# Performance work log

Hardware: AMD Instinct MI355X
Metric: run time of the kernel (lower is better)

## Reference

```python
import jax, jax.numpy as jnp
import numpy as np

NUM_LONGTERM_MEM = 16  # config.num_longterm_mem


def setup_inputs() -> dict:
    key = jax.random.key(0)
    ks = jax.random.split(key, 9)
    B, T, C, H = 32, 2048, 768, 1536
    s = 0.02
    return {
        "x": jax.random.normal(ks[0], (B, T, C), jnp.float32),
        "Wq": jax.random.normal(ks[1], (C, C), jnp.float32) * s,
        "bq": jax.random.normal(ks[2], (C,), jnp.float32) * s,
        "W0": jax.random.normal(ks[3], (B, H, C), jnp.float32) * s,
        "b0": jax.random.normal(ks[4], (B, H), jnp.float32) * s,
        "W1": jax.random.normal(ks[5], (B, C, H), jnp.float32) * s,
        "b1": jax.random.normal(ks[6], (B, C), jnp.float32) * s,
        "Wo": jax.random.normal(ks[7], (C, C), jnp.float32) * s,
        "bo": jax.random.normal(ks[8], (C,), jnp.float32) * s,
    }


def reference(x, Wq, bq, W0, b0, W1, b1, Wo, bo):
    # x: [B, T, C]. Per-sample memory MLP weights W0 [B,H,C], W1 [B,C,H].
    B, T, C = x.shape
    L = NUM_LONGTERM_MEM
    # query projection (nn.Linear: x @ W^T + b)
    q = jnp.einsum("btc,dc->btd", x, Wq) + bq                       # [B,T,C]
    # per-sample 2-layer memory MLP with SiLU
    h = jax.nn.silu(jnp.einsum("btc,bhc->bth", q, W0) + b0[:, None, :])  # [B,T,H]
    mem = jnp.einsum("bth,bch->btc", h, W1) + b1[:, None, :]        # [B,T,C]
    # adaptive_avg_pool1d over T -> L (T divisible by L => uniform window mean)
    pooled = mem.reshape(B, L, T // L, C).mean(axis=2)              # [B,L,C]
    # output projection
    return jnp.einsum("blc,dc->bld", pooled, Wo) + bo               # [B,L,C]
```

## Files before the change

kernel.cpp:

```cpp
#include <hip/hip_runtime.h>
#include <stdint.h>

#define B_ 32
#define T_ 2048
#define C_ 768
#define H_ 1536
#define L_ 16

typedef unsigned short u16;
typedef __bf16 bf16x8 __attribute__((ext_vector_type(8)));
typedef float f32x4 __attribute__((ext_vector_type(4)));

__device__ __forceinline__ u16 f2bf(float f) {
    union { float f; uint32_t u; } v; v.f = f;
    uint32_t r = (v.u + 0x7fffu + ((v.u >> 16) & 1u)) >> 16;
    return (u16)r;
}

__device__ __forceinline__ float wave_sum(float v) {
    v += __shfl_xor(v, 1);  v += __shfl_xor(v, 2);  v += __shfl_xor(v, 4);
    v += __shfl_xor(v, 8);  v += __shfl_xor(v, 16); v += __shfl_xor(v, 32);
    return v;
}

__global__ void k_cvt(const float* __restrict__ in, u16* __restrict__ out, int n4) {
    int stride = gridDim.x * blockDim.x;
    for (int i = blockIdx.x * blockDim.x + threadIdx.x; i < n4; i += stride) {
        float4 v = reinterpret_cast<const float4*>(in)[i];
        ushort4 o;
        o.x = f2bf(v.x); o.y = f2bf(v.y); o.z = f2bf(v.z); o.w = f2bf(v.w);
        reinterpret_cast<ushort4*>(out)[i] = o;
    }
}

__device__ __forceinline__ void gload16(const u16* g, u16* l) {
    __builtin_amdgcn_global_load_lds((const __attribute__((address_space(1))) void*)g,
                                     (__attribute__((address_space(3))) void*)l, 16, 0, 0);
}

#define PH_SYNC() do { __builtin_amdgcn_s_barrier(); \
    asm volatile("s_waitcnt lgkmcnt(0)" ::: "memory"); \
    __builtin_amdgcn_sched_barrier(0); } while (0)
#define PH_END() do { __builtin_amdgcn_sched_barrier(0); __builtin_amdgcn_s_barrier(); } while (0)

template <int EPI>
__global__ __launch_bounds__(512, 2) void k_gemm8(const u16* __restrict__ Aall,
                                                  const u16* __restrict__ Ball,
                                                  const float* __restrict__ biasall,
                                                  u16* __restrict__ qout,
                                                  float* __restrict__ ph) {
    __shared__ u16 sm[65536];
    const int t = threadIdx.x;
    const int w = t >> 6, lane = t & 63;
    const int wr = w >> 2, wc = w & 3;
    const int l15 = lane & 15, kq = lane >> 4, cx = lane & 7;

    const int n0 = blockIdx.x * 256;
    const int m0 = blockIdx.y * 256;
    const u16* A; const u16* Bm; const float* bias;
    if constexpr (EPI == 0) {
        A = Aall + (size_t)m0 * C_;
        Bm = Ball + (size_t)n0 * C_;
        bias = biasall + n0;
    } else {
        const int b = blockIdx.z;
        A = Aall + ((size_t)b * T_ + m0) * C_;
        Bm = Ball + ((size_t)b * H_ + n0) * C_;
        bias = biasall + (size_t)b * H_ + n0;
    }

    const int rl = (w << 4) + (lane >> 3);
    const int cs = (((lane & 7) ^ ((lane >> 3) & 7)) << 3);
    const int ldst = (w << 10);

    auto stA = [&](int kt, int h) {
        const u16* g = A + (size_t)(h * 128 + rl) * C_ + kt * 64 + cs;
        u16* l = sm + (kt & 1) * 32768 + h * 8192 + ldst;
        gload16(g, l);
        gload16(g + 8 * C_, l + 512);
    };
    auto stB = [&](int kt, int h) {
        const u16* g = Bm + (size_t)(h * 128 + rl) * C_ + kt * 64 + cs;
        u16* l = sm + (kt & 1) * 32768 + 16384 + h * 8192 + ldst;
        gload16(g, l);
        gload16(g + 8 * C_, l + 512);
    };

    f32x4 acc[8][4];
#pragma unroll
    for (int m = 0; m < 8; ++m)
#pragma unroll
        for (int n = 0; n < 4; ++n) acc[m][n] = (f32x4){0.f, 0.f, 0.f, 0.f};

    bf16x8 a0[4][2], a1[4][2], bfr[2][2];

    auto rdA = [&](bf16x8 (&a)[4][2], int bt, int mq) {
        const u16* Ah = sm + bt * 32768 + wr * 8192;
#pragma unroll
        for (int mm = 0; mm < 4; ++mm) {
            const u16* rp = Ah + ((mq * 4 + mm) * 16 + l15) * 64;
#pragma unroll
            for (int ks = 0; ks < 2; ++ks)
                a[mm][ks] = *reinterpret_cast<const bf16x8*>(rp + ((((ks << 2) + kq) ^ cx) << 3));
        }
    };
    auto rdB = [&](int bt, int qn) {
        const u16* Bh = sm + bt * 32768 + 16384 + (wc >> 1) * 8192;
        const int cb = (wc & 1) * 64 + qn * 32;
#pragma unroll
        for (int nn = 0; nn < 2; ++nn) {
            const u16* cp = Bh + (cb + nn * 16 + l15) * 64;
#pragma unroll
            for (int ks = 0; ks < 2; ++ks)
                bfr[nn][ks] = *reinterpret_cast<const bf16x8*>(cp + ((((ks << 2) + kq) ^ cx) << 3));
        }
    };
    auto mma16 = [&](bf16x8 (&a)[4][2], int mq, int qn) {
        __builtin_amdgcn_s_setprio(1);
#pragma unroll
        for (int ks = 0; ks < 2; ++ks)
#pragma unroll
            for (int mm = 0; mm < 4; ++mm)
#pragma unroll
                for (int nn = 0; nn < 2; ++nn)
                    acc[mq * 4 + mm][qn * 2 + nn] = __builtin_amdgcn_mfma_f32_16x16x32_bf16(
                        a[mm][ks], bfr[nn][ks], acc[mq * 4 + mm][qn * 2 + nn], 0, 0, 0);
        __builtin_amdgcn_s_setprio(0);
    };

    stA(0, 0); stA(0, 1); stB(0, 0); stB(0, 1);
    stA(1, 0); stA(1, 1);
    asm volatile("s_waitcnt vmcnt(4)" ::: "memory");
    __builtin_amdgcn_s_barrier();

#pragma unroll 1
    for (int kt = 0; kt < 12; ++kt) {
        const int bt = kt & 1;
        rdA(a0, bt, 0);
        rdB(bt, 0);
        if (kt + 1 < 12) stB(kt + 1, 0);
        PH_SYNC();
        mma16(a0, 0, 0);
        PH_END();
        rdA(a1, bt, 1);
        if (kt + 1 < 12) stB(kt + 1, 1);
        PH_SYNC();
        mma16(a1, 1, 0);
        PH_END();
        rdB(bt, 1);
        if (kt + 2 < 12) stA(kt + 2, 0);
        PH_SYNC();
        mma16(a0, 0, 1);
        PH_END();
        if (kt + 2 < 12) {
            stA(kt + 2, 1);
            asm volatile("s_waitcnt vmcnt(4)" ::: "memory");
        } else {
            asm volatile("s_waitcnt vmcnt(0)" ::: "memory");
        }
        __builtin_amdgcn_s_barrier();
        __builtin_amdgcn_sched_barrier(0);
        mma16(a1, 1, 1);
        PH_END();
    }

    if constexpr (EPI == 0) {
        const int colb = n0 + wc * 64 + l15;
        const int rowb = m0 + wr * 128 + (kq << 2);
#pragma unroll
        for (int n = 0; n < 4; ++n) {
            float bv = bias[wc * 64 + n * 16 + l15];
            int c = colb + n * 16;
#pragma unroll
            for (int m = 0; m < 8; ++m)
#pragma unroll
                for (int r = 0; r < 4; ++r)
                    qout[(size_t)(rowb + m * 16 + r) * C_ + c] = f2bf(acc[m][n][r] + bv);
        }
    } else {
        const int b = blockIdx.z;
        const int lwin = blockIdx.y * 2 + wr;
#pragma unroll
        for (int n = 0; n < 4; ++n) {
            int cloc = wc * 64 + n * 16 + l15;
            float bv = bias[cloc];
            float s = 0.f;
#pragma unroll
            for (int m = 0; m < 8; ++m)
#pragma unroll
                for (int r = 0; r < 4; ++r) {
                    float v = acc[m][n][r] + bv;
                    s += v / (1.f + __expf(-v));
                }
            s += __shfl_xor(s, 16);
            s += __shfl_xor(s, 32);
            if (kq == 0)
                ph[((size_t)b * L_ + lwin) * H_ + n0 + cloc] = s * (1.f / 128.f);
        }
    }
}

__device__ __forceinline__ void stage_bf16_gload(const u16* gtile, int ld, u16* Ts,
                                                 int w, int lane) {
    const int r_in = lane >> 3;
    const int c0   = (lane & 7) << 3;
#pragma unroll
    for (int j = 0; j < 4; ++j) {
        int row = ((w << 2) + j) * 8 + r_in;
        const u16* g = gtile + (size_t)row * ld + c0;
        u16* l = Ts + (((w << 2) + j) << 9);
        gload16(g, l);
    }
}

__device__ __forceinline__ void stage_f32_cvt(const float* gtile, int ld, u16* Ts, int t) {
#pragma unroll
    for (int i = 0; i < 8; ++i) {
        int slot = t + (i << 8);
        int row  = slot >> 4;
        int c4   = (slot & 15) << 2;
        float4 v = *reinterpret_cast<const float4*>(gtile + (size_t)row * ld + c4);
        ushort4 o;
        o.x = f2bf(v.x); o.y = f2bf(v.y); o.z = f2bf(v.z); o.w = f2bf(v.w);
        *reinterpret_cast<ushort4*>(&Ts[row * 64 + c4]) = o;
    }
}

__device__ __forceinline__ void mfma_tile(const u16* As, const u16* Bs,
                                          f32x4 (&acc)[4][4], int wr, int wc, int lane) {
#pragma unroll
    for (int ks = 0; ks < 2; ++ks) {
        const int ko = (ks << 5) + ((lane >> 4) << 3);
        bf16x8 a[4], b[4];
#pragma unroll
        for (int m = 0; m < 4; ++m)
            a[m] = *reinterpret_cast<const bf16x8*>(&As[(wr * 64 + m * 16 + (lane & 15)) * 64 + ko]);
#pragma unroll
        for (int n = 0; n < 4; ++n)
            b[n] = *reinterpret_cast<const bf16x8*>(&Bs[(wc * 64 + n * 16 + (lane & 15)) * 64 + ko]);
#pragma unroll
        for (int m = 0; m < 4; ++m)
#pragma unroll
            for (int n = 0; n < 4; ++n)
                acc[m][n] = __builtin_amdgcn_mfma_f32_16x16x32_bf16(a[m], b[n], acc[m][n], 0, 0, 0);
    }
}

__global__ __launch_bounds__(256, 2) void k_gemm1(const float* __restrict__ x,
                                                  const u16* __restrict__ Wqb,
                                                  const float* __restrict__ bq,
                                                  u16* __restrict__ qb) {
    __shared__ u16 As[128 * 64];
    __shared__ u16 Bs[128 * 64];
    const int t = threadIdx.x, w = t >> 6, lane = t & 63;
    const int wr = w >> 1, wc = w & 1;
    const int m0 = blockIdx.y * 128;
    const int n0 = blockIdx.x * 128;

    f32x4 acc[4][4];
#pragma unroll
    for (int m = 0; m < 4; ++m)
#pragma unroll
        for (int n = 0; n < 4; ++n) acc[m][n] = (f32x4){0.f, 0.f, 0.f, 0.f};

    for (int kt = 0; kt < C_ / 64; ++kt) {
        stage_f32_cvt(x + (size_t)m0 * C_ + kt * 64, C_, As, t);
        stage_bf16_gload(Wqb + (size_t)n0 * C_ + kt * 64, C_, Bs, w, lane);
        __syncthreads();
        mfma_tile(As, Bs, acc, wr, wc, lane);
        __syncthreads();
    }

    const int r0 = m0 + wr * 64 + ((lane >> 4) << 2);
    const int cb = n0 + wc * 64 + (lane & 15);
#pragma unroll
    for (int n = 0; n < 4; ++n) {
        int c = cb + n * 16;
        float bb = bq[c];
#pragma unroll
        for (int m = 0; m < 4; ++m)
#pragma unroll
            for (int r = 0; r < 4; ++r)
                qb[(size_t)(r0 + m * 16 + r) * C_ + c] = f2bf(acc[m][n][r] + bb);
    }
}

template <bool BPRE>
__global__ __launch_bounds__(256, 2) void k_gemm2(const u16* __restrict__ qb,
                                                  const u16* __restrict__ W0b,
                                                  const float* __restrict__ W0f,
                                                  const float* __restrict__ b0,
                                                  float* __restrict__ ph) {
    __shared__ u16 As[128 * 64];
    __shared__ u16 Bs[128 * 64];
    __shared__ float Ps[2][128];
    const int t = threadIdx.x, w = t >> 6, lane = t & 63;
    const int wr = w >> 1, wc = w & 1;
    const int b  = blockIdx.z;
    const int mt = blockIdx.y;
    const int n0 = blockIdx.x * 128;
    const u16* Abase = qb + ((size_t)b * T_ + mt * 128) * C_;

    f32x4 acc[4][4];
#pragma unroll
    for (int m = 0; m < 4; ++m)
#pragma unroll
        for (int n = 0; n < 4; ++n) acc[m][n] = (f32x4){0.f, 0.f, 0.f, 0.f};

    for (int kt = 0; kt < C_ / 64; ++kt) {
        stage_bf16_gload(Abase + kt * 64, C_, As, w, lane);
        if (BPRE)
            stage_bf16_gload(W0b + ((size_t)b * H_ + n0) * C_ + kt * 64, C_, Bs, w, lane);
        else
            stage_f32_cvt(W0f + ((size_t)b * H_ + n0) * C_ + kt * 64, C_, Bs, t);
        __syncthreads();
        mfma_tile(As, Bs, acc, wr, wc, lane);
        __syncthreads();
    }

    float s[4];
#pragma unroll
    for (int n = 0; n < 4; ++n) {
        int c = n0 + wc * 64 + n * 16 + (lane & 15);
        float bb = b0[b * H_ + c];
        float sum = 0.f;
#pragma unroll
        for (int m = 0; m < 4; ++m)
#pragma unroll
            for (int r = 0; r < 4; ++r) {
                float v = acc[m][n][r] + bb;
                sum += v / (1.f + __expf(-v));
            }
        sum += __shfl_xor(sum, 16);
        sum += __shfl_xor(sum, 32);
        s[n] = sum;
    }
    if (lane < 16) {
#pragma unroll
        for (int n = 0; n < 4; ++n) Ps[wr][wc * 64 + n * 16 + lane] = s[n];
    }
    __syncthreads();
    if (t < 128)
        ph[((size_t)b * L_ + mt) * H_ + n0 + t] = (Ps[0][t] + Ps[1][t]) * (1.f / 128.f);
}

__global__ __launch_bounds__(256) void k_3a(const float* __restrict__ ph,
                                            const float* __restrict__ W1,
                                            const float* __restrict__ b1,
                                            float* __restrict__ pooled) {
    const int t = threadIdx.x, w = t >> 6, lane = t & 63;
    const int b  = blockIdx.y;
    const int cb = blockIdx.x * 16 + w * 4;

    float acc[4][16];
#pragma unroll
    for (int g = 0; g < 4; ++g)
#pragma unroll
        for (int l = 0; l < 16; ++l) acc[g][l] = 0.f;

    for (int i = 0; i < H_ / 256; ++i) {
        int h0 = i * 256 + lane * 4;
        float4 wv[4];
#pragma unroll
        for (int g = 0; g < 4; ++g)
            wv[g] = *reinterpret_cast<const float4*>(W1 + ((size_t)b * C_ + cb + g) * H_ + h0);
#pragma unroll
        for (int l = 0; l < 16; ++l) {
            float4 pv = *reinterpret_cast<const float4*>(ph + ((size_t)b * L_ + l) * H_ + h0);
#pragma unroll
            for (int g = 0; g < 4; ++g)
                acc[g][l] += wv[g].x * pv.x + wv[g].y * pv.y + wv[g].z * pv.z + wv[g].w * pv.w;
        }
    }
#pragma unroll
    for (int g = 0; g < 4; ++g)
#pragma unroll
        for (int l = 0; l < 16; ++l) acc[g][l] = wave_sum(acc[g][l]);

    if (lane < 16) {
#pragma unroll
        for (int g = 0; g < 4; ++g)
            pooled[((size_t)b * L_ + lane) * C_ + cb + g] = acc[g][lane] + b1[b * C_ + cb + g];
    }
}

__global__ __launch_bounds__(256) void k_3b(const float* __restrict__ pooled,
                                            const float* __restrict__ Wo,
                                            const float* __restrict__ bo,
                                            float* __restrict__ out) {
    __shared__ __align__(16) float ps[4 * 768];
    const int t = threadIdx.x, w = t >> 6, lane = t & 63;
    const int rr0 = blockIdx.x * 4;

    for (int idx = t; idx < 4 * 768; idx += 256)
        ps[idx] = pooled[(size_t)rr0 * 768 + idx];
    __syncthreads();

    for (int d = w; d < 768; d += 4) {
        float a0 = 0.f, a1 = 0.f, a2 = 0.f, a3 = 0.f;
#pragma unroll
        for (int i = 0; i < 3; ++i) {
            int c = i * 256 + lane * 4;
            float4 wv = *reinterpret_cast<const float4*>(Wo + (size_t)d * 768 + c);
            float4 p0 = *reinterpret_cast<const float4*>(&ps[0 * 768 + c]);
            float4 p1 = *reinterpret_cast<const float4*>(&ps[1 * 768 + c]);
            float4 p2 = *reinterpret_cast<const float4*>(&ps[2 * 768 + c]);
            float4 p3 = *reinterpret_cast<const float4*>(&ps[3 * 768 + c]);
            a0 += wv.x * p0.x + wv.y * p0.y + wv.z * p0.z + wv.w * p0.w;
            a1 += wv.x * p1.x + wv.y * p1.y + wv.z * p1.z + wv.w * p1.w;
            a2 += wv.x * p2.x + wv.y * p2.y + wv.z * p2.z + wv.w * p2.w;
            a3 += wv.x * p3.x + wv.y * p3.y + wv.z * p3.z + wv.w * p3.w;
        }
        a0 = wave_sum(a0); a1 = wave_sum(a1); a2 = wave_sum(a2); a3 = wave_sum(a3);
        if (lane == 0) {
            float bb = bo[d];
            out[(size_t)(rr0 + 0) * 768 + d] = a0 + bb;
            out[(size_t)(rr0 + 1) * 768 + d] = a1 + bb;
            out[(size_t)(rr0 + 2) * 768 + d] = a2 + bb;
            out[(size_t)(rr0 + 3) * 768 + d] = a3 + bb;
        }
    }
}

extern "C" void kernel_launch(void* const* d_in, const int* in_sizes, int n_in,
                              void* d_out, int out_size, void* d_ws, size_t ws_size,
                              hipStream_t stream) {
    const float* x  = (const float*)d_in[0];
    const float* Wq = (const float*)d_in[1];
    const float* bq = (const float*)d_in[2];
    const float* W0 = (const float*)d_in[3];
    const float* b0 = (const float*)d_in[4];
    const float* W1 = (const float*)d_in[5];
    const float* b1 = (const float*)d_in[6];
    const float* Wo = (const float*)d_in[7];
    const float* bo = (const float*)d_in[8];
    float* out = (float*)d_out;

    char* p = (char*)d_ws;
    size_t off = 0;
    auto carve = [&](size_t bytes) -> char* {
        char* r = p + off;
        off += (bytes + 255) & ~(size_t)255;
        return r;
    };
    u16*   qb     = (u16*)carve((size_t)B_ * T_ * C_ * 2);
    u16*   Wqb    = (u16*)carve((size_t)C_ * C_ * 2);
    float* ph     = (float*)carve((size_t)B_ * L_ * H_ * 4);
    float* pooled = (float*)carve((size_t)B_ * L_ * C_ * 4);

    const size_t xb_bytes  = (size_t)B_ * T_ * C_ * 2;
    const size_t w0b_bytes = (size_t)B_ * H_ * C_ * 2;

    if (off + xb_bytes <= ws_size) {
        u16* xb  = (u16*)carve(xb_bytes);
        u16* W0b = xb;

        k_cvt<<<dim3(2048), 256, 0, stream>>>(x, xb, B_ * T_ * C_ / 4);
        k_cvt<<<dim3(64), 256, 0, stream>>>(Wq, Wqb, C_ * C_ / 4);
        k_gemm8<0><<<dim3(C_ / 256, (B_ * T_) / 256), 512, 0, stream>>>(xb, Wqb, bq, qb, nullptr);
        k_cvt<<<dim3(2048), 256, 0, stream>>>(W0, W0b, B_ * H_ * C_ / 4);
        k_gemm8<1><<<dim3(H_ / 256, T_ / 256, B_), 512, 0, stream>>>(qb, W0b, b0, nullptr, ph);
    } else {
        u16* W0b = nullptr;
        if (off + w0b_bytes <= ws_size) W0b = (u16*)carve(w0b_bytes);

        k_cvt<<<dim3(64), 256, 0, stream>>>(Wq, Wqb, C_ * C_ / 4);
        if (W0b)
            k_cvt<<<dim3(2048), 256, 0, stream>>>(W0, W0b, B_ * H_ * C_ / 4);
        k_gemm1<<<dim3(C_ / 128, (B_ * T_) / 128), 256, 0, stream>>>(x, Wqb, bq, qb);
        if (W0b)
            k_gemm2<true><<<dim3(H_ / 128, L_, B_), 256, 0, stream>>>(qb, W0b, nullptr, b0, ph);
        else
            k_gemm2<false><<<dim3(H_ / 128, L_, B_), 256, 0, stream>>>(qb, nullptr, W0, b0, ph);
    }

    k_3a<<<dim3(C_ / 16, B_), 256, 0, stream>>>(ph, W1, b1, pooled);
    k_3b<<<dim3(B_ * L_ / 4), 256, 0, stream>>>(pooled, Wo, bo, out);
}
```

Before: 667.1 us.

## Remap workgroups across XCDs and prefetch B tile one phase earlier

```diff
diff --git a/kernel.cpp b/kernel.cpp
--- a/kernel.cpp
+++ b/kernel.cpp
@@ -55,18 +55,26 @@
     const int wr = w >> 2, wc = w & 3;
     const int l15 = lane & 15, kq = lane >> 4, cx = lane & 7;
 
-    const int n0 = blockIdx.x * 256;
-    const int m0 = blockIdx.y * 256;
+    const int gx = gridDim.x, gy = gridDim.y;
+    const int nwg = gx * gy * gridDim.z;
+    int flat = blockIdx.x + gx * (blockIdx.y + gy * blockIdx.z);
+    if ((nwg & 7) == 0) flat = (flat & 7) * (nwg >> 3) + (flat >> 3);
+    const int bx = flat % gx;
+    const int tmp = flat / gx;
+    const int by = tmp % gy;
+    const int bz = tmp / gy;
+
+    const int n0 = bx * 256;
+    const int m0 = by * 256;
     const u16* A; const u16* Bm; const float* bias;
     if constexpr (EPI == 0) {
         A = Aall + (size_t)m0 * C_;
         Bm = Ball + (size_t)n0 * C_;
         bias = biasall + n0;
     } else {
-        const int b = blockIdx.z;
-        A = Aall + ((size_t)b * T_ + m0) * C_;
-        Bm = Ball + ((size_t)b * H_ + n0) * C_;
-        bias = biasall + (size_t)b * H_ + n0;
+        A = Aall + ((size_t)bz * T_ + m0) * C_;
+        Bm = Ball + ((size_t)bz * H_ + n0) * C_;
+        bias = biasall + (size_t)bz * H_ + n0;
     }
 
     const int rl = (w << 4) + (lane >> 3);
@@ -129,8 +137,8 @@
     };
 
     stA(0, 0); stA(0, 1); stB(0, 0); stB(0, 1);
-    stA(1, 0); stA(1, 1);
-    asm volatile("s_waitcnt vmcnt(4)" ::: "memory");
+    stA(1, 0); stA(1, 1); stB(1, 0);
+    asm volatile("s_waitcnt vmcnt(6)" ::: "memory");
     __builtin_amdgcn_s_barrier();
 
 #pragma unroll 1
@@ -138,12 +146,11 @@
         const int bt = kt & 1;
         rdA(a0, bt, 0);
         rdB(bt, 0);
-        if (kt + 1 < 12) stB(kt + 1, 0);
+        if (kt + 1 < 12) stB(kt + 1, 1);
         PH_SYNC();
         mma16(a0, 0, 0);
         PH_END();
         rdA(a1, bt, 1);
-        if (kt + 1 < 12) stB(kt + 1, 1);
         PH_SYNC();
         mma16(a1, 1, 0);
         PH_END();
@@ -154,7 +161,8 @@
         PH_END();
         if (kt + 2 < 12) {
             stA(kt + 2, 1);
-            asm volatile("s_waitcnt vmcnt(4)" ::: "memory");
+            stB(kt + 2, 0);
+            asm volatile("s_waitcnt vmcnt(6)" ::: "memory");
         } else {
             asm volatile("s_waitcnt vmcnt(0)" ::: "memory");
         }
@@ -167,19 +175,20 @@
     if constexpr (EPI == 0) {
         const int colb = n0 + wc * 64 + l15;
         const int rowb = m0 + wr * 128 + (kq << 2);
-#pragma unroll
-        for (int n = 0; n < 4; ++n) {
-            float bv = bias[wc * 64 + n * 16 + l15];
-            int c = colb + n * 16;
-#pragma unroll
-            for (int m = 0; m < 8; ++m)
-#pragma unroll
-                for (int r = 0; r < 4; ++r)
-                    qout[(size_t)(rowb + m * 16 + r) * C_ + c] = f2bf(acc[m][n][r] + bv);
-        }
+        float bv[4];
+#pragma unroll
+        for (int n = 0; n < 4; ++n) bv[n] = bias[wc * 64 + n * 16 + l15];
+#pragma unroll
+        for (int m = 0; m < 8; ++m)
+#pragma unroll
+            for (int r = 0; r < 4; ++r) {
+                size_t ro = (size_t)(rowb + m * 16 + r) * C_;
+#pragma unroll
+                for (int n = 0; n < 4; ++n)
+                    qout[ro + colb + n * 16] = f2bf(acc[m][n][r] + bv[n]);
+            }
     } else {
-        const int b = blockIdx.z;
-        const int lwin = blockIdx.y * 2 + wr;
+        const int lwin = by * 2 + wr;
 #pragma unroll
         for (int n = 0; n < 4; ++n) {
             int cloc = wc * 64 + n * 16 + l15;
@@ -195,7 +204,7 @@
             s += __shfl_xor(s, 16);
             s += __shfl_xor(s, 32);
             if (kq == 0)
-                ph[((size_t)b * L_ + lwin) * H_ + n0 + cloc] = s * (1.f / 128.f);
+                ph[((size_t)bz * L_ + lwin) * H_ + n0 + cloc] = s * (1.f / 128.f);
         }
     }
 }
```

Measured after the change: 647.6 us. -2.9%, faster.
